# Optimization experiments

Hardware: AMD Instinct MI355X
Metric: run time of the kernel (lower is better)

Reference implementation:

```python
import jax, jax.numpy as jnp
import numpy as np

B, C, H, W = 8, 64, 256, 512
FOV = np.pi / 4.0
KH = KW = 3


def _sphere_indices(H, W, fov):
    """Nearest-neighbor gather indices for a 3x3 spherical (gnomonic) kernel
    of angular extent `fov` on an equirectangular grid. Returns int32 [H, W, 9]."""
    taps = [(p, q) for p in (-1, 0, 1) for q in (-1, 0, 1)]
    theta = (0.5 - (np.arange(H) + 0.5) / H) * np.pi            # latitude per row [H]
    phi = ((np.arange(W) + 0.5) / W - 0.5) * 2.0 * np.pi        # longitude per col [W]
    r = np.tan(fov / 2.0)                                       # tangent-plane half extent
    gi_l, gj_l = [], []
    for (p, q) in taps:
        y_t, x_t = p * r, q * r
        rho = np.hypot(x_t, y_t)
        if rho == 0.0:
            lat = theta
            lon_off = np.zeros_like(theta)
        else:
            nu = np.arctan(rho)
            lat = np.arcsin(np.clip(np.cos(nu) * np.sin(theta)
                                    + y_t * np.sin(nu) * np.cos(theta) / rho, -1.0, 1.0))
            lon_off = np.arctan2(x_t * np.sin(nu),
                                 rho * np.cos(theta) * np.cos(nu)
                                 - y_t * np.sin(theta) * np.sin(nu))
        lon = phi[None, :] + lon_off[:, None]                   # [H, W]
        gi = np.clip(np.round((0.5 - lat / np.pi) * H - 0.5), 0, H - 1).astype(np.int32)
        gi = np.broadcast_to(gi[:, None], (H, W)).copy()
        gj = (np.round((lon / (2.0 * np.pi) + 0.5) * W - 0.5).astype(np.int64) % W).astype(np.int32)
        gi_l.append(gi)
        gj_l.append(gj)
    return np.stack(gi_l, axis=-1), np.stack(gj_l, axis=-1)    # [H, W, 9] each


def setup_inputs() -> dict:
    key = jax.random.key(0)
    k1, k2 = jax.random.split(key)
    feature = jax.random.normal(k1, (B, C, H, W), dtype=jnp.float32)
    weight = jax.random.normal(k2, (1, C, KH, KW), dtype=jnp.float32) * 0.05
    gi, gj = _sphere_indices(H, W, FOV)
    return {"feature": feature, "weight": weight,
            "gi": jnp.asarray(gi), "gj": jnp.asarray(gj)}


def reference(feature, weight, gi, gj):
    # SphericalConv: gather-based 3x3 conv over spherical sampling grid, stride 1, no bias.
    O, Cc, kh, kw = weight.shape
    wflat = weight.reshape(O, Cc, kh * kw)                      # [O, C, 9]
    Bb = feature.shape[0]
    Hh, Ww = gi.shape[0], gi.shape[1]
    out = jnp.zeros((Bb, O, Hh, Ww), feature.dtype)
    for k in range(kh * kw):                                    # fixed 9-tap loop
        xk = feature[:, :, gi[:, :, k], gj[:, :, k]]            # gather -> [B, C, H, W]
        out = out + jnp.einsum('bchw,oc->bohw', xk, wflat[:, :, k])
    # nn.Upsample(scale_factor=2) default nearest
    return jnp.repeat(jnp.repeat(out, 2, axis=2), 2, axis=3)
```

## Files before the change

### kernel.cpp

```cpp
#include <hip/hip_runtime.h>

#define Bn   8
#define Cn   64
#define Hn   256
#define Wn   512
#define HWn  (Hn * Wn)
#define TAPS 9

__global__ __launch_bounds__(256) void pass0_idx(
    const int* __restrict__ gi, const int* __restrict__ gj,
    int* __restrict__ off9)
{
    int p = blockIdx.x * 256 + threadIdx.x;
    int base = p * TAPS;
#pragma unroll
    for (int k = 0; k < TAPS; ++k)
        off9[k * HWn + p] = gi[base + k] * Wn + gj[base + k];
}

__global__ __launch_bounds__(256) void pass1_chandot(
    const float* __restrict__ feat, const float* __restrict__ wt,
    float* __restrict__ D)
{
    __shared__ float wl[Cn * TAPS];
    for (int i = threadIdx.x; i < Cn * TAPS; i += 256) wl[i] = wt[i];
    __syncthreads();

    int p = blockIdx.x * 256 + threadIdx.x;

    float acc[TAPS][Bn];
#pragma unroll
    for (int k = 0; k < TAPS; ++k)
#pragma unroll
        for (int b = 0; b < Bn; ++b) acc[k][b] = 0.f;

#pragma unroll 2
    for (int c = 0; c < Cn; ++c) {
        float f[Bn];
#pragma unroll
        for (int b = 0; b < Bn; ++b)
            f[b] = feat[((size_t)b * Cn + c) * HWn + p];
#pragma unroll
        for (int k = 0; k < TAPS; ++k) {
            float wv = wl[c * TAPS + k];
#pragma unroll
            for (int b = 0; b < Bn; ++b)
                acc[k][b] = fmaf(f[b], wv, acc[k][b]);
        }
    }

#pragma unroll
    for (int k = 0; k < TAPS; ++k) {
        float4* dst = (float4*)(D + ((size_t)k * HWn + p) * Bn);
        dst[0] = make_float4(acc[k][0], acc[k][1], acc[k][2], acc[k][3]);
        dst[1] = make_float4(acc[k][4], acc[k][5], acc[k][6], acc[k][7]);
    }
}

__global__ __launch_bounds__(256) void pass2_gather(
    const float* __restrict__ D, const int* __restrict__ off9,
    float* __restrict__ out)
{
    int p = blockIdx.x * 256 + threadIdx.x;
    int w = p & (Wn - 1);
    int h = p >> 9;

    float4 a0 = make_float4(0.f, 0.f, 0.f, 0.f);
    float4 a1 = make_float4(0.f, 0.f, 0.f, 0.f);
#pragma unroll
    for (int k = 0; k < TAPS; ++k) {
        int off = off9[k * HWn + p];
        const float4* d = (const float4*)(D + ((size_t)k * HWn + off) * Bn);
        float4 d0 = d[0], d1 = d[1];
        a0.x += d0.x; a0.y += d0.y; a0.z += d0.z; a0.w += d0.w;
        a1.x += d1.x; a1.y += d1.y; a1.z += d1.z; a1.w += d1.w;
    }

    float vals[Bn] = {a0.x, a0.y, a0.z, a0.w, a1.x, a1.y, a1.z, a1.w};
#pragma unroll
    for (int b = 0; b < Bn; ++b) {
        float2 vv = make_float2(vals[b], vals[b]);
        size_t o = ((size_t)b * (2 * Hn) + 2 * h) * (size_t)(2 * Wn) + 2 * w;
        *(float2*)(out + o)            = vv;
        *(float2*)(out + o + 2 * Wn)   = vv;
    }
}

__global__ __launch_bounds__(256) void direct_kernel(
    const float* __restrict__ feat, const float* __restrict__ wt,
    const int* __restrict__ gi, const int* __restrict__ gj,
    float* __restrict__ out)
{
    int p = blockIdx.x * blockDim.x + threadIdx.x;
    int w = p & (Wn - 1);
    int h = (p >> 9) & (Hn - 1);
    int b = p >> 17;

    int iidx = ((h << 9) | w) * TAPS;
    int off[TAPS];
#pragma unroll
    for (int k = 0; k < TAPS; ++k)
        off[k] = gi[iidx + k] * Wn + gj[iidx + k];

    float acc = 0.f;
    for (int c = 0; c < Cn; ++c) {
        const float* fc = feat + ((size_t)b * Cn + c) * HWn;
#pragma unroll
        for (int k = 0; k < TAPS; ++k)
            acc = fmaf(fc[off[k]], wt[c * TAPS + k], acc);
    }

    float2 v = make_float2(acc, acc);
    size_t o0 = ((size_t)b * (2 * Hn) + 2 * h) * (size_t)(2 * Wn) + 2 * w;
    *(float2*)(out + o0)          = v;
    *(float2*)(out + o0 + 2 * Wn) = v;
}

extern "C" void kernel_launch(void* const* d_in, const int* in_sizes, int n_in,
                              void* d_out, int out_size, void* d_ws, size_t ws_size,
                              hipStream_t stream) {
    const float* feat = (const float*)d_in[0];
    const float* wt   = (const float*)d_in[1];
    const int*   gi   = (const int*)d_in[2];
    const int*   gj   = (const int*)d_in[3];
    float*       out  = (float*)d_out;

    const size_t bytesD   = (size_t)TAPS * HWn * Bn * sizeof(float);
    const size_t bytesOff = (size_t)TAPS * HWn * sizeof(int);

    if (ws_size >= bytesD + bytesOff) {
        float* D    = (float*)d_ws;
        int*   off9 = (int*)((char*)d_ws + bytesD);
        pass0_idx    <<<HWn / 256, 256, 0, stream>>>(gi, gj, off9);
        pass1_chandot<<<HWn / 256, 256, 0, stream>>>(feat, wt, D);
        pass2_gather <<<HWn / 256, 256, 0, stream>>>(D, off9, out);
    } else {
        direct_kernel<<<(Bn * HWn) / 256, 256, 0, stream>>>(feat, wt, gi, gj, out);
    }
}
```

Before: 406.0 us.

## Fold index pass into gather, prefetch channels, use nontemporal loads/stores

Removes the separate index-precompute kernel: the gather kernel now stages each block's gi/gj into shared memory with coalesced loads and computes the offsets there, saving one launch and the off9 round-trip through global memory. The channel-dot kernel drops the shared-memory weight table in favour of uniform global weight reads. It also software-pipelines feature loads in groups of four channels with double buffering, using nontemporal loads. Output stores become nontemporal. The risks are higher register pressure from the prefetch buffers plus the 9x8 accumulators, and possible occupancy loss.

```diff
diff --git a/kernel.cpp b/kernel.cpp
--- a/kernel.cpp
+++ b/kernel.cpp
@@ -7,26 +7,13 @@
 #define HWn  (Hn * Wn)
 #define TAPS 9
 
-__global__ __launch_bounds__(256) void pass0_idx(
-    const int* __restrict__ gi, const int* __restrict__ gj,
-    int* __restrict__ off9)
-{
-    int p = blockIdx.x * 256 + threadIdx.x;
-    int base = p * TAPS;
-#pragma unroll
-    for (int k = 0; k < TAPS; ++k)
-        off9[k * HWn + p] = gi[base + k] * Wn + gj[base + k];
-}
+typedef float vfloat2 __attribute__((ext_vector_type(2)));
 
 __global__ __launch_bounds__(256) void pass1_chandot(
     const float* __restrict__ feat, const float* __restrict__ wt,
     float* __restrict__ D)
 {
-    __shared__ float wl[Cn * TAPS];
-    for (int i = threadIdx.x; i < Cn * TAPS; i += 256) wl[i] = wt[i];
-    __syncthreads();
-
-    int p = blockIdx.x * 256 + threadIdx.x;
+    const int p = blockIdx.x * 256 + threadIdx.x;
 
     float acc[TAPS][Bn];
 #pragma unroll
@@ -34,18 +21,37 @@
 #pragma unroll
         for (int b = 0; b < Bn; ++b) acc[k][b] = 0.f;
 
-#pragma unroll 2
-    for (int c = 0; c < Cn; ++c) {
-        float f[Bn];
+    float buf[2][4][Bn];
+
+#pragma unroll
+    for (int ci = 0; ci < 4; ++ci)
 #pragma unroll
         for (int b = 0; b < Bn; ++b)
-            f[b] = feat[((size_t)b * Cn + c) * HWn + p];
+            buf[0][ci][b] = __builtin_nontemporal_load(
+                feat + (size_t)(b * Cn + ci) * HWn + p);
+
 #pragma unroll
-        for (int k = 0; k < TAPS; ++k) {
-            float wv = wl[c * TAPS + k];
+    for (int g = 0; g < 16; ++g) {
+        const int cur = g & 1, nxt = cur ^ 1;
+        if (g < 15) {
+            const int c0 = (g + 1) * 4;
 #pragma unroll
-            for (int b = 0; b < Bn; ++b)
-                acc[k][b] = fmaf(f[b], wv, acc[k][b]);
+            for (int ci = 0; ci < 4; ++ci)
+#pragma unroll
+                for (int b = 0; b < Bn; ++b)
+                    buf[nxt][ci][b] = __builtin_nontemporal_load(
+                        feat + (size_t)(b * Cn + c0 + ci) * HWn + p);
+        }
+#pragma unroll
+        for (int ci = 0; ci < 4; ++ci) {
+            const int c = g * 4 + ci;
+#pragma unroll
+            for (int k = 0; k < TAPS; ++k) {
+                const float wv = wt[c * TAPS + k];
+#pragma unroll
+                for (int b = 0; b < Bn; ++b)
+                    acc[k][b] = fmaf(buf[cur][ci][b], wv, acc[k][b]);
+            }
         }
     }
 
@@ -58,31 +64,42 @@
 }
 
 __global__ __launch_bounds__(256) void pass2_gather(
-    const float* __restrict__ D, const int* __restrict__ off9,
-    float* __restrict__ out)
+    const float* __restrict__ D, const int* __restrict__ gi,
+    const int* __restrict__ gj, float* __restrict__ out)
 {
-    int p = blockIdx.x * 256 + threadIdx.x;
-    int w = p & (Wn - 1);
-    int h = p >> 9;
+    __shared__ int loff[256 * TAPS];
+    const int tid   = threadIdx.x;
+    const int p0    = blockIdx.x * 256;
+    const int gbase = p0 * TAPS;
 
-    float4 a0 = make_float4(0.f, 0.f, 0.f, 0.f);
-    float4 a1 = make_float4(0.f, 0.f, 0.f, 0.f);
+#pragma unroll
+    for (int i = tid; i < 256 * TAPS; i += 256)
+        loff[i] = gi[gbase + i] * Wn + gj[gbase + i];
+    __syncthreads();
+
+    const int p = p0 + tid;
+    const int w = p & (Wn - 1);
+    const int h = p >> 9;
+
+    float a[Bn];
+#pragma unroll
+    for (int b = 0; b < Bn; ++b) a[b] = 0.f;
+
 #pragma unroll
     for (int k = 0; k < TAPS; ++k) {
-        int off = off9[k * HWn + p];
+        const int off = loff[tid * TAPS + k];
         const float4* d = (const float4*)(D + ((size_t)k * HWn + off) * Bn);
         float4 d0 = d[0], d1 = d[1];
-        a0.x += d0.x; a0.y += d0.y; a0.z += d0.z; a0.w += d0.w;
-        a1.x += d1.x; a1.y += d1.y; a1.z += d1.z; a1.w += d1.w;
+        a[0] += d0.x; a[1] += d0.y; a[2] += d0.z; a[3] += d0.w;
+        a[4] += d1.x; a[5] += d1.y; a[6] += d1.z; a[7] += d1.w;
     }
 
-    float vals[Bn] = {a0.x, a0.y, a0.z, a0.w, a1.x, a1.y, a1.z, a1.w};
 #pragma unroll
     for (int b = 0; b < Bn; ++b) {
-        float2 vv = make_float2(vals[b], vals[b]);
+        vfloat2 vv = {a[b], a[b]};
         size_t o = ((size_t)b * (2 * Hn) + 2 * h) * (size_t)(2 * Wn) + 2 * w;
-        *(float2*)(out + o)            = vv;
-        *(float2*)(out + o + 2 * Wn)   = vv;
+        __builtin_nontemporal_store(vv, (vfloat2*)(out + o));
+        __builtin_nontemporal_store(vv, (vfloat2*)(out + o + 2 * Wn));
     }
 }
 
@@ -125,15 +142,12 @@
     const int*   gj   = (const int*)d_in[3];
     float*       out  = (float*)d_out;
 
-    const size_t bytesD   = (size_t)TAPS * HWn * Bn * sizeof(float);
-    const size_t bytesOff = (size_t)TAPS * HWn * sizeof(int);
+    const size_t bytesD = (size_t)TAPS * HWn * Bn * sizeof(float);
 
-    if (ws_size >= bytesD + bytesOff) {
-        float* D    = (float*)d_ws;
-        int*   off9 = (int*)((char*)d_ws + bytesD);
-        pass0_idx    <<<HWn / 256, 256, 0, stream>>>(gi, gj, off9);
+    if (ws_size >= bytesD) {
+        float* D = (float*)d_ws;
         pass1_chandot<<<HWn / 256, 256, 0, stream>>>(feat, wt, D);
-        pass2_gather <<<HWn / 256, 256, 0, stream>>>(D, off9, out);
+        pass2_gather <<<HWn / 256, 256, 0, stream>>>(D, gi, gj, out);
     } else {
         direct_kernel<<<(Bn * HWn) / 256, 256, 0, stream>>>(feat, wt, gi, gj, out);
     }
```

Result: faster. 364.9 us (-10.1%).
